# Performance work log

Hardware: AMD Instinct MI355X
Metric: run time of the kernel (lower is better)

The kernel has to match this reference:

```python
import jax, jax.numpy as jnp
import numpy as np

B, L, D, H = 2, 8192, 1024, 16
HD = D // H  # head_dim = 64


def setup_inputs() -> dict:
    key = jax.random.key(0)
    ks = jax.random.split(key, 5)
    s = 1.0 / np.sqrt(D)
    return {
        "x": jax.random.normal(ks[0], (B, L, D), dtype=jnp.float32),
        "Wq": jax.random.normal(ks[1], (D, D), dtype=jnp.float32) * s,
        "bq": jnp.zeros((D,), dtype=jnp.float32),
        "Wk": jax.random.normal(ks[2], (D, D), dtype=jnp.float32) * s,
        "bk": jnp.zeros((D,), dtype=jnp.float32),
        "Wv": jax.random.normal(ks[3], (D, D), dtype=jnp.float32) * s,
        "bv": jnp.zeros((D,), dtype=jnp.float32),
        "Wo": jax.random.normal(ks[4], (D, D), dtype=jnp.float32) * s,
        "bo": jnp.zeros((D,), dtype=jnp.float32),
    }


def _rotary(seq_len, dim):
    pos = jnp.arange(seq_len, dtype=jnp.float32)
    freq = 1.0 / (10000.0 ** (jnp.arange(0, dim, 2, dtype=jnp.float32) / dim))
    ang = pos[:, None] * freq[None, :]               # (L, dim/2)
    sin, cos = jnp.sin(ang), jnp.cos(ang)
    # interleave-duplicate: stack((s,s),-1).reshape(L,dim)  (matches torch code)
    sin = jnp.stack((sin, sin), axis=-1).reshape(seq_len, dim)
    cos = jnp.stack((cos, cos), axis=-1).reshape(seq_len, dim)
    return sin, cos


def _rotate_half(t):
    t1, t2 = jnp.split(t, 2, axis=-1)
    return jnp.concatenate([-t2, t1], axis=-1)


def reference(x, Wq, bq, Wk, bk, Wv, bv, Wo, bo):
    b, l, d = x.shape
    q = (x @ Wq + bq).reshape(b, l, H, HD)
    k = (x @ Wk + bk).reshape(b, l, H, HD)
    v = (x @ Wv + bv).reshape(b, l, H, HD)

    sin, cos = _rotary(l, HD)
    sin = sin[None, :, None, :]  # (1, L, 1, HD)
    cos = cos[None, :, None, :]
    q = q * cos + _rotate_half(q) * sin
    k = k * cos + _rotate_half(k) * sin

    # NOTE: faithful to original — heads NOT transposed to (B,H,L,HD),
    # so scores are (B, L, H, H): attention mixes across heads per position.
    scores = jnp.einsum('blhd,bled->blhe', q, k) / jnp.sqrt(jnp.float32(HD))
    w = jax.nn.softmax(scores, axis=-1)              # dropout = identity (eval)
    out = jnp.einsum('blhe,bled->blhd', w, v).reshape(b, l, d)
    return out @ Wo + bo
```

## Files before the change

### kernel.cpp

```cpp
#include <hip/hip_runtime.h>
#include <hip/hip_bf16.h>

typedef __bf16 bf16_t;
typedef __bf16 bf16x8 __attribute__((ext_vector_type(8)));
typedef float f32x4 __attribute__((ext_vector_type(4)));

#define SEQ_L 8192
#define DMODEL 1024
#define NHEAD 16
#define HDIM 64
static constexpr int MROWS = 2 * SEQ_L;

__device__ __forceinline__ void async_cp16(const bf16_t* g, bf16_t* l) {
  __builtin_amdgcn_global_load_lds(
      (__attribute__((address_space(1))) void*)(void*)(g),
      (__attribute__((address_space(3))) void*)(void*)(l), 16, 0, 0);
}
__device__ __forceinline__ void wg_barrier() { __builtin_amdgcn_s_barrier(); }

__global__ __launch_bounds__(256) void f32_to_bf16_k(const float* __restrict__ in,
                                                     bf16_t* __restrict__ out, int n) {
  int i = (blockIdx.x * 256 + threadIdx.x) * 8;
  if (i >= n) return;
  float4 a = *(const float4*)(in + i);
  float4 b = *(const float4*)(in + i + 4);
  bf16x8 o;
  o[0] = (__bf16)a.x; o[1] = (__bf16)a.y; o[2] = (__bf16)a.z; o[3] = (__bf16)a.w;
  o[4] = (__bf16)b.x; o[5] = (__bf16)b.y; o[6] = (__bf16)b.z; o[7] = (__bf16)b.w;
  *(bf16x8*)(out + i) = o;
}

__global__ __launch_bounds__(256) void w_to_bt_k(
    const float* __restrict__ W0, const float* __restrict__ W1,
    const float* __restrict__ W2, const float* __restrict__ W3,
    bf16_t* __restrict__ T0, bf16_t* __restrict__ T1,
    bf16_t* __restrict__ T2, bf16_t* __restrict__ T3) {
  __shared__ float tile[32][33];
  const int z = blockIdx.z;
  const float* W = (z == 0) ? W0 : (z == 1) ? W1 : (z == 2) ? W2 : W3;
  bf16_t* T = (z == 0) ? T0 : (z == 1) ? T1 : (z == 2) ? T2 : T3;
  const int bx = blockIdx.x, by = blockIdx.y;
  const int tx = threadIdx.x, ty = threadIdx.y;
#pragma unroll
  for (int r = 0; r < 4; ++r)
    tile[ty + r * 8][tx] = W[(size_t)(by * 32 + ty + r * 8) * DMODEL + bx * 32 + tx];
  __syncthreads();
#pragma unroll
  for (int r = 0; r < 4; ++r)
    T[(size_t)(bx * 32 + ty + r * 8) * DMODEL + by * 32 + tx] = (bf16_t)tile[tx][ty + r * 8];
}

__global__ __launch_bounds__(256) void rope_tab_k(float2* __restrict__ tab) {
  int i = blockIdx.x * 256 + threadIdx.x;
  int pos = i >> 5, j = i & 31;
  double freq = pow(10000.0, -(double)j / 32.0);
  double ang = (double)pos * freq;
  tab[i] = make_float2((float)cos(ang), (float)sin(ang));
}

template <int MODE>
__global__ __launch_bounds__(512, 2) void gemm256(
    const bf16_t* __restrict__ A, const bf16_t* __restrict__ Bt,
    const float* __restrict__ b0, const float* __restrict__ b1,
    const float* __restrict__ b2, const float2* __restrict__ rope,
    void* __restrict__ O0, void* __restrict__ O1, void* __restrict__ O2) {
  constexpr int K = DMODEL;
  constexpr int KT = K / 64;
  __shared__ bf16_t As_[2][256 * 64];
  __shared__ bf16_t Bs_[2][256 * 64];
  const int tid = threadIdx.x;
  const int lane = tid & 63;
  const int wave = tid >> 6;
  const int wm = wave >> 2;
  const int wn = wave & 3;
  const size_t row0 = (size_t)blockIdx.x * 256;
  const int col0 = blockIdx.y * 256;
  const int fr = lane & 15;
  const int fkb = (lane >> 4) * 16;

  const int srow = tid >> 3;
  const int schunk = (tid & 7) ^ ((tid >> 3) & 7);
  const bf16_t* gA = A + (row0 + srow) * K + schunk * 8;
  const bf16_t* gB = Bt + ((size_t)col0 + srow) * K + schunk * 8;

#define STAGE_A(j, h)                                  \
  do {                                                 \
    const bf16_t* _g = gA + ((h)*128) * K + (j)*64;    \
    bf16_t* _l = &As_[(j)&1][(h)*8192 + tid * 8];      \
    async_cp16(_g, _l);                                \
    async_cp16(_g + 64 * K, _l + 4096);                \
  } while (0)
#define STAGE_B(j, h)                                  \
  do {                                                 \
    const bf16_t* _g = gB + ((h)*128) * K + (j)*64;    \
    bf16_t* _l = &Bs_[(j)&1][(h)*8192 + tid * 8];      \
    async_cp16(_g, _l);                                \
    async_cp16(_g + 64 * K, _l + 4096);                \
  } while (0)
#define STAGE_T(j)                                     \
  do {                                                 \
    STAGE_A(j, 0); STAGE_A(j, 1);                      \
    STAGE_B(j, 0); STAGE_B(j, 1);                      \
  } while (0)
#define RD(base, row, kh)                                                    \
  (*(const bf16x8*)((const char*)(base) +                                    \
                    (((row)*128 + ((kh)*64 + fkb)) ^ (((row)&7) << 4))))
#define VMCNT(n) asm volatile("s_waitcnt vmcnt(" #n ")")
#define SCHED_FENCE() __builtin_amdgcn_sched_barrier(0)

  f32x4 acc[8][4] = {};
  bf16x8 a0[4][2], a1[4][2], bfr[4][2];

  STAGE_T(0);
  STAGE_T(1);
  VMCNT(8);
  wg_barrier();
  SCHED_FENCE();

  for (int m = 0; m < KT; ++m) {
    const bf16_t* Ac = &As_[m & 1][0];
    const bf16_t* Bc = &Bs_[m & 1][0];
#pragma unroll
    for (int f = 0; f < 4; ++f) {
      const int r = wn * 64 + f * 16 + fr;
      bfr[f][0] = RD(Bc, r, 0);
      bfr[f][1] = RD(Bc, r, 1);
    }
#pragma unroll
    for (int f = 0; f < 4; ++f) {
      const int r = wm * 128 + f * 16 + fr;
      a0[f][0] = RD(Ac, r, 0);
      a0[f][1] = RD(Ac, r, 1);
    }
#pragma unroll
    for (int f = 0; f < 4; ++f) {
      const int r = wm * 128 + (4 + f) * 16 + fr;
      a1[f][0] = RD(Ac, r, 0);
      a1[f][1] = RD(Ac, r, 1);
    }
    __builtin_amdgcn_s_setprio(1);
#pragma unroll
    for (int f = 0; f < 4; ++f)
#pragma unroll
      for (int n = 0; n < 4; ++n)
#pragma unroll
        for (int kh = 0; kh < 2; ++kh)
          acc[f][n] = __builtin_amdgcn_mfma_f32_16x16x32_bf16(a0[f][kh], bfr[n][kh], acc[f][n], 0, 0, 0);
#pragma unroll
    for (int f = 0; f < 4; ++f)
#pragma unroll
      for (int n = 0; n < 4; ++n)
#pragma unroll
        for (int kh = 0; kh < 2; ++kh)
          acc[4 + f][n] = __builtin_amdgcn_mfma_f32_16x16x32_bf16(a1[f][kh], bfr[n][kh], acc[4 + f][n], 0, 0, 0);
    __builtin_amdgcn_s_setprio(0);
    wg_barrier();
    SCHED_FENCE();
    if (m + 2 < KT) {
      STAGE_T(m + 2);
      VMCNT(8);
    } else {
      VMCNT(0);
    }
    wg_barrier();
    SCHED_FENCE();
  }
#undef STAGE_A
#undef STAGE_B
#undef STAGE_T
#undef RD
#undef VMCNT
#undef SCHED_FENCE

  const int lr = (lane >> 4) * 4;
  const int lc = lane & 15;
  const int gcol = col0 + wn * 64;
  int which = 0;
  const float* bias = b0;
  int ocol = gcol;
  if constexpr (MODE == 0) {
    which = gcol >> 10;
    bias = (which == 0) ? b0 : (which == 1) ? b1 : b2;
    ocol = gcol - (which << 10);
  }
  const bool do_rope = (MODE == 0) && (which < 2);
  bf16_t* Cb = nullptr;
  float* Cf = nullptr;
  if constexpr (MODE == 0)
    Cb = (bf16_t*)((which == 0) ? O0 : (which == 1) ? O1 : O2);
  else
    Cf = (float*)O0;

#pragma unroll
  for (int mf = 0; mf < 8; ++mf) {
#pragma unroll
    for (int i = 0; i < 4; ++i) {
      const size_t grow = row0 + wm * 128 + mf * 16 + lr + i;
      float vv[4];
#pragma unroll
      for (int n = 0; n < 4; ++n) vv[n] = acc[mf][n][i] + bias[ocol + n * 16 + lc];
      if (do_rope) {
        const int pos = (int)(grow & (size_t)(SEQ_L - 1));
        const float2* rp = rope + (size_t)pos * 32 + (lc >> 1);
        float rv[4];
#pragma unroll
        for (int n = 0; n < 4; ++n) {
          float2 cs = rp[n * 8];
          rv[n] = (n < 2) ? vv[n] * cs.x - vv[n + 2] * cs.y
                          : vv[n] * cs.x + vv[n - 2] * cs.y;
        }
#pragma unroll
        for (int n = 0; n < 4; ++n) vv[n] = rv[n];
      }
      const size_t cbase = grow * (size_t)DMODEL + ocol + lc;
      if constexpr (MODE == 1) {
#pragma unroll
        for (int n = 0; n < 4; ++n) Cf[cbase + n * 16] = vv[n];
      } else {
#pragma unroll
        for (int n = 0; n < 4; ++n) Cb[cbase + n * 16] = (bf16_t)vv[n];
      }
    }
  }
}

__global__ __launch_bounds__(256) void attn_heads_k(const bf16_t* __restrict__ qb,
                                                    const bf16_t* __restrict__ kb,
                                                    const bf16_t* __restrict__ vb,
                                                    bf16_t* __restrict__ ob) {
  const int t = blockIdx.x * 256 + threadIdx.x;
  const int row = t >> 4;
  const int h = t & 15;
  const size_t rbase = (size_t)row * DMODEL;

  float q[HDIM];
#pragma unroll
  for (int j = 0; j < 8; ++j) {
    bf16x8 v8 = *(const bf16x8*)(qb + rbase + h * HDIM + j * 8);
#pragma unroll
    for (int u = 0; u < 8; ++u) q[j * 8 + u] = (float)v8[u];
  }
  float s[NHEAD];
#pragma unroll
  for (int e = 0; e < NHEAD; ++e) {
    float a = 0.f;
#pragma unroll
    for (int j = 0; j < 8; ++j) {
      bf16x8 k8 = *(const bf16x8*)(kb + rbase + e * HDIM + j * 8);
#pragma unroll
      for (int u = 0; u < 8; ++u) a += q[j * 8 + u] * (float)k8[u];
    }
    s[e] = a * 0.125f;
  }
  float mx = s[0];
#pragma unroll
  for (int e = 1; e < NHEAD; ++e) mx = fmaxf(mx, s[e]);
  float sum = 0.f;
#pragma unroll
  for (int e = 0; e < NHEAD; ++e) {
    s[e] = __expf(s[e] - mx);
    sum += s[e];
  }
  const float inv = 1.f / sum;
  float o[HDIM] = {};
#pragma unroll
  for (int e = 0; e < NHEAD; ++e) {
    const float w = s[e] * inv;
#pragma unroll
    for (int j = 0; j < 8; ++j) {
      bf16x8 v8 = *(const bf16x8*)(vb + rbase + e * HDIM + j * 8);
#pragma unroll
      for (int u = 0; u < 8; ++u) o[j * 8 + u] += w * (float)v8[u];
    }
  }
#pragma unroll
  for (int j = 0; j < 8; ++j) {
    bf16x8 st;
#pragma unroll
    for (int u = 0; u < 8; ++u) st[u] = (__bf16)o[j * 8 + u];
    *(bf16x8*)(ob + rbase + h * HDIM + j * 8) = st;
  }
}

extern "C" void kernel_launch(void* const* d_in, const int* in_sizes, int n_in,
                              void* d_out, int out_size, void* d_ws, size_t ws_size,
                              hipStream_t stream) {
  const float* x = (const float*)d_in[0];
  const float* Wq = (const float*)d_in[1];
  const float* bq = (const float*)d_in[2];
  const float* Wk = (const float*)d_in[3];
  const float* bk = (const float*)d_in[4];
  const float* Wv = (const float*)d_in[5];
  const float* bv = (const float*)d_in[6];
  const float* Wo = (const float*)d_in[7];
  const float* bo = (const float*)d_in[8];

  const int M = MROWS, N = DMODEL, K = DMODEL;

  char* p = (char*)d_ws;
  bf16_t* xb = (bf16_t*)p;    p += (size_t)M * K * 2;
  bf16_t* Wqkvt = (bf16_t*)p; p += (size_t)3 * N * K * 2;
  bf16_t* Wot = (bf16_t*)p;   p += (size_t)N * K * 2;
  bf16_t* qb = (bf16_t*)p;    p += (size_t)M * N * 2;
  bf16_t* kb = (bf16_t*)p;    p += (size_t)M * N * 2;
  bf16_t* vb = (bf16_t*)p;    p += (size_t)M * N * 2;
  bf16_t* ab = (bf16_t*)p;    p += (size_t)M * N * 2;
  float2* rope = (float2*)p;  p += (size_t)SEQ_L * 32 * sizeof(float2);

  bf16_t* Wqt = Wqkvt;
  bf16_t* Wkt = Wqkvt + (size_t)N * K;
  bf16_t* Wvt = Wqkvt + (size_t)2 * N * K;

  f32_to_bf16_k<<<(M * K) / (256 * 8), 256, 0, stream>>>(x, xb, M * K);
  w_to_bt_k<<<dim3(32, 32, 4), dim3(32, 8), 0, stream>>>(Wq, Wk, Wv, Wo, Wqt, Wkt, Wvt, Wot);
  rope_tab_k<<<(SEQ_L * 32) / 256, 256, 0, stream>>>(rope);

  gemm256<0><<<dim3(M / 256, (3 * N) / 256), 512, 0, stream>>>(
      xb, Wqkvt, bq, bk, bv, rope, (void*)qb, (void*)kb, (void*)vb);
  attn_heads_k<<<(M * NHEAD) / 256, 256, 0, stream>>>(qb, kb, vb, ab);
  gemm256<1><<<dim3(M / 256, N / 256), 512, 0, stream>>>(
      ab, Wot, bo, nullptr, nullptr, nullptr, d_out, nullptr, nullptr);
}
```

Baseline: 245.6 us.

## Shrink GEMM tiles to 128x128 with single-buffered LDS and 4 blocks per CU

Replaces the 256x256, 512-thread, double-buffered GEMM with a 128x128, 256-thread kernel that keeps one LDS buffer and allows 4 blocks per CU. The aim is to rely on occupancy across blocks to hide latency and to launch more blocks for better CU balance. Each k-step now waits for the next tile's global load to finish before compute, so in-block prefetch overlap is lost. Smaller tiles also lower data reuse and raise global and L2 traffic.

```diff
diff --git a/kernel.cpp b/kernel.cpp
--- a/kernel.cpp
+++ b/kernel.cpp
@@ -59,117 +59,94 @@
 }
 
 template <int MODE>
-__global__ __launch_bounds__(512, 2) void gemm256(
+__global__ __launch_bounds__(256, 4) void gemm128(
     const bf16_t* __restrict__ A, const bf16_t* __restrict__ Bt,
     const float* __restrict__ b0, const float* __restrict__ b1,
     const float* __restrict__ b2, const float2* __restrict__ rope,
     void* __restrict__ O0, void* __restrict__ O1, void* __restrict__ O2) {
   constexpr int K = DMODEL;
   constexpr int KT = K / 64;
-  __shared__ bf16_t As_[2][256 * 64];
-  __shared__ bf16_t Bs_[2][256 * 64];
+  __shared__ bf16_t As_[128 * 64];
+  __shared__ bf16_t Bs_[128 * 64];
   const int tid = threadIdx.x;
   const int lane = tid & 63;
   const int wave = tid >> 6;
-  const int wm = wave >> 2;
-  const int wn = wave & 3;
-  const size_t row0 = (size_t)blockIdx.x * 256;
-  const int col0 = blockIdx.y * 256;
+  const int wm = wave >> 1;
+  const int wn = wave & 1;
+  const size_t row0 = (size_t)blockIdx.x * 128;
+  const int col0 = blockIdx.y * 128;
   const int fr = lane & 15;
   const int fkb = (lane >> 4) * 16;
 
-  const int srow = tid >> 3;
-  const int schunk = (tid & 7) ^ ((tid >> 3) & 7);
-  const bf16_t* gA = A + (row0 + srow) * K + schunk * 8;
-  const bf16_t* gB = Bt + ((size_t)col0 + srow) * K + schunk * 8;
-
-#define STAGE_A(j, h)                                  \
-  do {                                                 \
-    const bf16_t* _g = gA + ((h)*128) * K + (j)*64;    \
-    bf16_t* _l = &As_[(j)&1][(h)*8192 + tid * 8];      \
-    async_cp16(_g, _l);                                \
-    async_cp16(_g + 64 * K, _l + 4096);                \
-  } while (0)
-#define STAGE_B(j, h)                                  \
-  do {                                                 \
-    const bf16_t* _g = gB + ((h)*128) * K + (j)*64;    \
-    bf16_t* _l = &Bs_[(j)&1][(h)*8192 + tid * 8];      \
-    async_cp16(_g, _l);                                \
-    async_cp16(_g + 64 * K, _l + 4096);                \
-  } while (0)
-#define STAGE_T(j)                                     \
-  do {                                                 \
-    STAGE_A(j, 0); STAGE_A(j, 1);                      \
-    STAGE_B(j, 0); STAGE_B(j, 1);                      \
+  const int srow = lane >> 3;
+  const int schunk = (lane & 7) ^ (lane >> 3);
+  const bf16_t* gA = A + (row0 + wave * 32 + srow) * K + schunk * 8;
+  const bf16_t* gB = Bt + ((size_t)col0 + wave * 32 + srow) * K + schunk * 8;
+  bf16_t* lA = As_ + wave * 2048 + lane * 8;
+  bf16_t* lB = Bs_ + wave * 2048 + lane * 8;
+
+#define STAGE(j)                                           \
+  do {                                                     \
+    async_cp16(gA + (j)*64, lA);                           \
+    async_cp16(gA + 8 * K + (j)*64, lA + 512);             \
+    async_cp16(gA + 16 * K + (j)*64, lA + 1024);           \
+    async_cp16(gA + 24 * K + (j)*64, lA + 1536);           \
+    async_cp16(gB + (j)*64, lB);                           \
+    async_cp16(gB + 8 * K + (j)*64, lB + 512);             \
+    async_cp16(gB + 16 * K + (j)*64, lB + 1024);           \
+    async_cp16(gB + 24 * K + (j)*64, lB + 1536);           \
   } while (0)
 #define RD(base, row, kh)                                                    \
   (*(const bf16x8*)((const char*)(base) +                                    \
-                    (((row)*128 + ((kh)*64 + fkb)) ^ (((row)&7) << 4))))
+                    ((((row)*128) + ((kh)*64 + fkb)) ^ (((row)&7) << 4))))
 #define VMCNT(n) asm volatile("s_waitcnt vmcnt(" #n ")")
+#define LGKM0() asm volatile("s_waitcnt lgkmcnt(0)")
 #define SCHED_FENCE() __builtin_amdgcn_sched_barrier(0)
 
-  f32x4 acc[8][4] = {};
-  bf16x8 a0[4][2], a1[4][2], bfr[4][2];
-
-  STAGE_T(0);
-  STAGE_T(1);
-  VMCNT(8);
+  f32x4 acc[4][4] = {};
+  bf16x8 a4[4], b4[4];
+
+  STAGE(0);
+  VMCNT(0);
   wg_barrier();
   SCHED_FENCE();
 
   for (int m = 0; m < KT; ++m) {
-    const bf16_t* Ac = &As_[m & 1][0];
-    const bf16_t* Bc = &Bs_[m & 1][0];
-#pragma unroll
-    for (int f = 0; f < 4; ++f) {
-      const int r = wn * 64 + f * 16 + fr;
-      bfr[f][0] = RD(Bc, r, 0);
-      bfr[f][1] = RD(Bc, r, 1);
-    }
-#pragma unroll
-    for (int f = 0; f < 4; ++f) {
-      const int r = wm * 128 + f * 16 + fr;
-      a0[f][0] = RD(Ac, r, 0);
-      a0[f][1] = RD(Ac, r, 1);
-    }
-#pragma unroll
-    for (int f = 0; f < 4; ++f) {
-      const int r = wm * 128 + (4 + f) * 16 + fr;
-      a1[f][0] = RD(Ac, r, 0);
-      a1[f][1] = RD(Ac, r, 1);
-    }
+#pragma unroll
+    for (int f = 0; f < 4; ++f) a4[f] = RD(As_, wm * 64 + f * 16 + fr, 0);
+#pragma unroll
+    for (int n = 0; n < 4; ++n) b4[n] = RD(Bs_, wn * 64 + n * 16 + fr, 0);
     __builtin_amdgcn_s_setprio(1);
 #pragma unroll
     for (int f = 0; f < 4; ++f)
 #pragma unroll
       for (int n = 0; n < 4; ++n)
-#pragma unroll
-        for (int kh = 0; kh < 2; ++kh)
-          acc[f][n] = __builtin_amdgcn_mfma_f32_16x16x32_bf16(a0[f][kh], bfr[n][kh], acc[f][n], 0, 0, 0);
+        acc[f][n] = __builtin_amdgcn_mfma_f32_16x16x32_bf16(a4[f], b4[n], acc[f][n], 0, 0, 0);
+    __builtin_amdgcn_s_setprio(0);
+#pragma unroll
+    for (int f = 0; f < 4; ++f) a4[f] = RD(As_, wm * 64 + f * 16 + fr, 1);
+#pragma unroll
+    for (int n = 0; n < 4; ++n) b4[n] = RD(Bs_, wn * 64 + n * 16 + fr, 1);
+    __builtin_amdgcn_s_setprio(1);
 #pragma unroll
     for (int f = 0; f < 4; ++f)
 #pragma unroll
       for (int n = 0; n < 4; ++n)
-#pragma unroll
-        for (int kh = 0; kh < 2; ++kh)
-          acc[4 + f][n] = __builtin_amdgcn_mfma_f32_16x16x32_bf16(a1[f][kh], bfr[n][kh], acc[4 + f][n], 0, 0, 0);
+        acc[f][n] = __builtin_amdgcn_mfma_f32_16x16x32_bf16(a4[f], b4[n], acc[f][n], 0, 0, 0);
     __builtin_amdgcn_s_setprio(0);
+    LGKM0();
+    SCHED_FENCE();
     wg_barrier();
     SCHED_FENCE();
-    if (m + 2 < KT) {
-      STAGE_T(m + 2);
-      VMCNT(8);
-    } else {
-      VMCNT(0);
-    }
+    if (m + 1 < KT) STAGE(m + 1);
+    VMCNT(0);
     wg_barrier();
     SCHED_FENCE();
   }
-#undef STAGE_A
-#undef STAGE_B
-#undef STAGE_T
+#undef STAGE
 #undef RD
 #undef VMCNT
+#undef LGKM0
 #undef SCHED_FENCE
 
   const int lr = (lane >> 4) * 4;
@@ -192,10 +169,10 @@
     Cf = (float*)O0;
 
 #pragma unroll
-  for (int mf = 0; mf < 8; ++mf) {
+  for (int mf = 0; mf < 4; ++mf) {
 #pragma unroll
     for (int i = 0; i < 4; ++i) {
-      const size_t grow = row0 + wm * 128 + mf * 16 + lr + i;
+      const size_t grow = row0 + wm * 64 + mf * 16 + lr + i;
       float vv[4];
 #pragma unroll
       for (int n = 0; n < 4; ++n) vv[n] = acc[mf][n][i] + bias[ocol + n * 16 + lc];
@@ -315,9 +292,9 @@
   w_to_bt_k<<<dim3(32, 32, 4), dim3(32, 8), 0, stream>>>(Wq, Wk, Wv, Wo, Wqt, Wkt, Wvt, Wot);
   rope_tab_k<<<(SEQ_L * 32) / 256, 256, 0, stream>>>(rope);
 
-  gemm256<0><<<dim3(M / 256, (3 * N) / 256), 512, 0, stream>>>(
+  gemm128<0><<<dim3(M / 128, (3 * N) / 128), 256, 0, stream>>>(
       xb, Wqkvt, bq, bk, bv, rope, (void*)qb, (void*)kb, (void*)vb);
   attn_heads_k<<<(M * NHEAD) / 256, 256, 0, stream>>>(qb, kb, vb, ab);
-  gemm256<1><<<dim3(M / 256, N / 256), 512, 0, stream>>>(
+  gemm128<1><<<dim3(M / 128, N / 128), 256, 0, stream>>>(
       ab, Wot, bo, nullptr, nullptr, nullptr, d_out, nullptr, nullptr);
 }
```

Result: faster. 230.5 us (-6.1%).
